# Kernel tuning notes

Hardware: AMD Instinct MI355X
Metric: run time of the kernel (lower is better)

Reference implementation:

```python
import jax, jax.numpy as jnp
import numpy as np

N_NODES = 200000
D = 512
N_EDGES = 12800000


def setup_inputs() -> dict:
    key = jax.random.key(0)
    k1, k2, k3 = jax.random.split(key, 3)
    x = jax.random.normal(k1, (N_NODES, D), dtype=jnp.float32)
    edge_index = jax.random.randint(k2, (2, N_EDGES), 0, N_NODES, dtype=jnp.int64)
    # GCNConv linear weight (glorot-ish scale) and bias
    W = jax.random.normal(k3, (D, 1), dtype=jnp.float32) / np.sqrt(D)
    b = jnp.zeros((1,), dtype=jnp.float32)
    return {"x": x, "edge_index": edge_index, "W": W, "b": b}


def reference(x, edge_index, W, b):
    """one_layer_gcn forward: GCNConv(d, 1) -> ReLU.

    Faithful to PyG GCNConv defaults: add self-loops, symmetric
    deg^{-1/2} normalization, linear transform first (out dim 1),
    scatter-add aggregation into target nodes, bias after aggregation.
    """
    n = x.shape[0]
    loop = jnp.arange(n, dtype=edge_index.dtype)
    src = jnp.concatenate([edge_index[0], loop])  # message sources (x_j)
    dst = jnp.concatenate([edge_index[1], loop])  # aggregation targets

    # degree of target nodes (with self-loops), symmetric normalization
    deg = jax.ops.segment_sum(jnp.ones_like(dst, dtype=x.dtype), dst, num_segments=n)
    dinv = jnp.where(deg > 0, jax.lax.rsqrt(deg), 0.0)
    norm = dinv[src] * dinv[dst]  # [E+N]

    h = x @ W  # [N, 1] -- trivial GEMM, out_channels = 1
    msg = h[src] * norm[:, None]  # gather + weight
    out = jax.ops.segment_sum(msg, dst, num_segments=n)  # scatter-add
    return jax.nn.relu(out + b)
```

## Files before the change

kernel.cpp:

```cpp
#include <hip/hip_runtime.h>


#define GCN_D 512
#define NPB 1024
#define NPB_SHIFT 10
#define CHUNK 8192
#define PT 512
#define CPAD 16

__global__ void init_cursor_kernel(int* __restrict__ cursor, int NB, int CAP) {
    int i = threadIdx.x;
    if (i < NB) cursor[i * CPAD] = i * CAP;
}

__global__ __launch_bounds__(PT) void place_kernel(const int* __restrict__ src,
                                                   const int* __restrict__ dst,
                                                   int* __restrict__ cursor,
                                                   unsigned int* __restrict__ packed,
                                                   int E, int NB, int CAP) {
    __shared__ unsigned int staging[CHUNK];
    __shared__ unsigned char bid[CHUNK];
    __shared__ int hist[256];
    __shared__ int lcur[256];
    __shared__ int delta[256];
    __shared__ int scanbuf[PT];

    const int tid = threadIdx.x;
    const int e0 = blockIdx.x * CHUNK;
    const int rem = min(CHUNK, E - e0);
    const int r4 = rem >> 2;

    const int4* d4p = reinterpret_cast<const int4*>(dst + e0);
    const int4* s4p = reinterpret_cast<const int4*>(src + e0);

    if (tid < 256) hist[tid] = 0;
    __syncthreads();

    int4 dreg[4];
    #pragma unroll
    for (int k = 0; k < 4; ++k) {
        int i4 = tid + k * PT;
        if (i4 < r4) {
            dreg[k] = d4p[i4];
            atomicAdd(&hist[dreg[k].x >> NPB_SHIFT], 1);
            atomicAdd(&hist[dreg[k].y >> NPB_SHIFT], 1);
            atomicAdd(&hist[dreg[k].z >> NPB_SHIFT], 1);
            atomicAdd(&hist[dreg[k].w >> NPB_SHIFT], 1);
        }
    }
    __syncthreads();

    int c = (tid < NB) ? hist[tid] : 0;
    scanbuf[tid] = c;
    for (int off = 1; off < 256; off <<= 1) {
        __syncthreads();
        int v = (tid >= off) ? scanbuf[tid - off] : 0;
        __syncthreads();
        scanbuf[tid] += v;
    }
    __syncthreads();
    if (tid < NB) {
        int ls = scanbuf[tid] - c;
        lcur[tid] = ls;
        if (c > 0)
            delta[tid] = atomicAdd(&cursor[tid * CPAD], c) - ls;
    }
    __syncthreads();

    #pragma unroll
    for (int k = 0; k < 4; ++k) {
        int i4 = tid + k * PT;
        if (i4 < r4) {
            int4 s4 = s4p[i4];
            int4 d = dreg[k];
            int b, pos;
            b = d.x >> NPB_SHIFT; pos = atomicAdd(&lcur[b], 1);
            staging[pos] = ((unsigned)s4.x << NPB_SHIFT) | (unsigned)(d.x & (NPB - 1));
            bid[pos] = (unsigned char)b;
            b = d.y >> NPB_SHIFT; pos = atomicAdd(&lcur[b], 1);
            staging[pos] = ((unsigned)s4.y << NPB_SHIFT) | (unsigned)(d.y & (NPB - 1));
            bid[pos] = (unsigned char)b;
            b = d.z >> NPB_SHIFT; pos = atomicAdd(&lcur[b], 1);
            staging[pos] = ((unsigned)s4.z << NPB_SHIFT) | (unsigned)(d.z & (NPB - 1));
            bid[pos] = (unsigned char)b;
            b = d.w >> NPB_SHIFT; pos = atomicAdd(&lcur[b], 1);
            staging[pos] = ((unsigned)s4.w << NPB_SHIFT) | (unsigned)(d.w & (NPB - 1));
            bid[pos] = (unsigned char)b;
        }
    }
    __syncthreads();

    for (int p = tid; p < rem; p += PT) {
        int b = bid[p];
        int op = p + delta[b];
        if (op < (b + 1) * CAP)
            packed[op] = staging[p];
    }
}

__global__ void gemv_kernel(const float* __restrict__ x, const float* __restrict__ W,
                            float* __restrict__ hprime, int n) {
    int wave = threadIdx.x >> 6;
    int lane = threadIdx.x & 63;
    int row = blockIdx.x * 4 + wave;
    if (row >= n) return;

    const float4* xr = reinterpret_cast<const float4*>(x + (size_t)row * GCN_D);
    const float4* Wv = reinterpret_cast<const float4*>(W);

    float4 a0 = xr[lane];
    float4 w0 = Wv[lane];
    float4 a1 = xr[lane + 64];
    float4 w1 = Wv[lane + 64];

    float dot = a0.x * w0.x + a0.y * w0.y + a0.z * w0.z + a0.w * w0.w
              + a1.x * w1.x + a1.y * w1.y + a1.z * w1.z + a1.w * w1.w;

    #pragma unroll
    for (int off = 32; off >= 1; off >>= 1)
        dot += __shfl_down(dot, off, 64);

    if (lane == 0) hprime[row] = dot;
}

__global__ __launch_bounds__(1024) void deg_hp_kernel(const unsigned int* __restrict__ packed,
                                                      const int* __restrict__ cursor,
                                                      int* __restrict__ deg,
                                                      float* __restrict__ hprime,
                                                      int N, int CAP) {
    int b = blockIdx.x;
    __shared__ int acc[NPB];
    for (int i = threadIdx.x; i < NPB; i += blockDim.x) acc[i] = 0;
    __syncthreads();
    int s0 = b * CAP;
    int s1 = min(cursor[b * CPAD], (b + 1) * CAP);
    int cnt = s1 - s0;
    int n4 = cnt >> 2;
    const uint4* p4 = reinterpret_cast<const uint4*>(packed + s0);
    for (int i = threadIdx.x; i < n4; i += blockDim.x) {
        uint4 p = p4[i];
        atomicAdd(&acc[p.x & (NPB - 1)], 1);
        atomicAdd(&acc[p.y & (NPB - 1)], 1);
        atomicAdd(&acc[p.z & (NPB - 1)], 1);
        atomicAdd(&acc[p.w & (NPB - 1)], 1);
    }
    if (threadIdx.x < (cnt & 3))
        atomicAdd(&acc[packed[s0 + (n4 << 2) + threadIdx.x] & (NPB - 1)], 1);
    __syncthreads();
    int node0 = b << NPB_SHIFT;
    for (int j = threadIdx.x; j < NPB; j += blockDim.x) {
        int node = node0 + j;
        if (node < N) {
            int dg = acc[j];
            deg[node] = dg;
            hprime[node] *= rsqrtf((float)(dg + 1));
        }
    }
}

__global__ __launch_bounds__(1024) void gather_kernel(const unsigned int* __restrict__ packed,
                                                      const int* __restrict__ cursor,
                                                      const float* __restrict__ hprime,
                                                      const int* __restrict__ deg,
                                                      const float* __restrict__ bias,
                                                      float* __restrict__ out,
                                                      int N, int CAP) {
    int b = blockIdx.x;
    __shared__ float acc[NPB];
    for (int i = threadIdx.x; i < NPB; i += blockDim.x) acc[i] = 0.f;
    __syncthreads();
    int s0 = b * CAP;
    int s1 = min(cursor[b * CPAD], (b + 1) * CAP);
    int cnt = s1 - s0;
    int n4 = cnt >> 2;
    const uint4* p4 = reinterpret_cast<const uint4*>(packed + s0);
    for (int i = threadIdx.x; i < n4; i += blockDim.x) {
        uint4 p = p4[i];
        atomicAdd(&acc[p.x & (NPB - 1)], hprime[p.x >> NPB_SHIFT]);
        atomicAdd(&acc[p.y & (NPB - 1)], hprime[p.y >> NPB_SHIFT]);
        atomicAdd(&acc[p.z & (NPB - 1)], hprime[p.z >> NPB_SHIFT]);
        atomicAdd(&acc[p.w & (NPB - 1)], hprime[p.w >> NPB_SHIFT]);
    }
    if (threadIdx.x < (cnt & 3)) {
        unsigned p = packed[s0 + (n4 << 2) + threadIdx.x];
        atomicAdd(&acc[p & (NPB - 1)], hprime[p >> NPB_SHIFT]);
    }
    __syncthreads();
    int node0 = b << NPB_SHIFT;
    float bb = bias[0];
    for (int j = threadIdx.x; j < NPB; j += blockDim.x) {
        int node = node0 + j;
        if (node < N) {
            float dinv = rsqrtf((float)(deg[node] + 1));
            float v = dinv * (acc[j] + hprime[node]) + bb;
            out[node] = v > 0.f ? v : 0.f;
        }
    }
}

__global__ void deg_kernel(const int* __restrict__ dst, int* __restrict__ deg, int e4) {
    int i = blockIdx.x * blockDim.x + threadIdx.x;
    if (i < e4) {
        int4 d = reinterpret_cast<const int4*>(dst)[i];
        atomicAdd(&deg[d.x], 1);
        atomicAdd(&deg[d.y], 1);
        atomicAdd(&deg[d.z], 1);
        atomicAdd(&deg[d.w], 1);
    }
}
__global__ void gemv_scaled_kernel(const float* __restrict__ x, const float* __restrict__ W,
                                   const int* __restrict__ deg, float* __restrict__ hprime, int n) {
    int wave = threadIdx.x >> 6;
    int lane = threadIdx.x & 63;
    int row = blockIdx.x * 4 + wave;
    if (row >= n) return;
    const float4* xr = reinterpret_cast<const float4*>(x + (size_t)row * GCN_D);
    const float4* Wv = reinterpret_cast<const float4*>(W);
    float4 a0 = xr[lane], w0 = Wv[lane];
    float4 a1 = xr[lane + 64], w1 = Wv[lane + 64];
    float dot = a0.x * w0.x + a0.y * w0.y + a0.z * w0.z + a0.w * w0.w
              + a1.x * w1.x + a1.y * w1.y + a1.z * w1.z + a1.w * w1.w;
    #pragma unroll
    for (int off = 32; off >= 1; off >>= 1) dot += __shfl_down(dot, off, 64);
    if (lane == 0) hprime[row] = dot * rsqrtf((float)(deg[row] + 1));
}
__global__ void scatter_kernel(const int* __restrict__ src, const int* __restrict__ dst,
                               const float* __restrict__ hprime, float* __restrict__ acc,
                               int e4) {
    int i = blockIdx.x * blockDim.x + threadIdx.x;
    if (i < e4) {
        int4 s = reinterpret_cast<const int4*>(src)[i];
        int4 d = reinterpret_cast<const int4*>(dst)[i];
        atomicAdd(&acc[d.x], hprime[s.x]);
        atomicAdd(&acc[d.y], hprime[s.y]);
        atomicAdd(&acc[d.z], hprime[s.z]);
        atomicAdd(&acc[d.w], hprime[s.w]);
    }
}
__global__ void final_kernel(const float* __restrict__ hprime, const float* __restrict__ acc,
                             const int* __restrict__ deg, const float* __restrict__ bptr,
                             float* __restrict__ out, int n) {
    int i = blockIdx.x * blockDim.x + threadIdx.x;
    if (i < n) {
        float dinv = rsqrtf((float)(deg[i] + 1));
        float v = dinv * (acc[i] + hprime[i]) + bptr[0];
        out[i] = v > 0.0f ? v : 0.0f;
    }
}

extern "C" void kernel_launch(void* const* d_in, const int* in_sizes, int n_in,
                              void* d_out, int out_size, void* d_ws, size_t ws_size,
                              hipStream_t stream) {
    const float* x    = (const float*)d_in[0];
    const int*   ei   = (const int*)d_in[1];
    const float* W    = (const float*)d_in[2];
    const float* bias = (const float*)d_in[3];
    float* out = (float*)d_out;

    const int n = in_sizes[0] / GCN_D;
    const int E = in_sizes[1] / 2;
    const int e4 = E / 4;

    const int* src = ei;
    const int* dst = ei + E;

    const int NB = (n + NPB - 1) >> NPB_SHIFT;

    auto align64 = [](size_t v) { return (v + 63) & ~(size_t)63; };
    size_t off_deg    = 0;
    size_t off_hprime = align64(off_deg    + (size_t)n * 4);
    size_t off_cursor = align64(off_hprime + (size_t)n * 4);
    size_t off_packed = align64(off_cursor + (size_t)NB * CPAD * 4);

    char* ws = (char*)d_ws;
    int*   deg    = (int*)(ws + off_deg);
    float* hprime = (float*)(ws + off_hprime);

    int CAP = 0;
    if (ws_size > off_packed) {
        size_t cap_avail = (ws_size - off_packed) / ((size_t)NB * 4);
        CAP = (int)(cap_avail > 131072 ? 131072 : cap_avail) & ~3;
    }
    const int mean_load = (int)(((long long)E + NB - 1) / NB);

    if (NB <= 256 && CAP >= mean_load + mean_load / 32) {
        int* cursor = (int*)(ws + off_cursor);
        unsigned int* packed = (unsigned int*)(ws + off_packed);

        init_cursor_kernel<<<1, 256, 0, stream>>>(cursor, NB, CAP);
        place_kernel<<<(E + CHUNK - 1) / CHUNK, PT, 0, stream>>>(src, dst, cursor, packed, E, NB, CAP);
        gemv_kernel<<<(n + 3) / 4, 256, 0, stream>>>(x, W, hprime, n);
        deg_hp_kernel<<<NB, 1024, 0, stream>>>(packed, cursor, deg, hprime, n, CAP);
        gather_kernel<<<NB, 1024, 0, stream>>>(packed, cursor, hprime, deg, bias, out, n, CAP);
    } else {
        float* acc = (float*)(ws + off_cursor);
        hipMemsetAsync(ws, 0, (size_t)3 * n * 4, stream);
        deg_kernel<<<(e4 + 255) / 256, 256, 0, stream>>>(dst, deg, e4);
        gemv_scaled_kernel<<<(n + 3) / 4, 256, 0, stream>>>(x, W, deg, hprime, n);
        scatter_kernel<<<(e4 + 255) / 256, 256, 0, stream>>>(src, dst, hprime, acc, e4);
        final_kernel<<<(n + 255) / 256, 256, 0, stream>>>(hprime, acc, deg, bias, out, n);
    }
}
```

Before: 249.3 us.

## Split bucket blocks across multiple CTAs and precompute placement indices in staging

The place kernel now stores each record's final global index alongside the payload in 64-bit shared staging, so the flush loop no longer looks up bucket deltas. It also uses smaller chunks with 256 threads. Degree counting and gathering now split each bucket across four 256-thread blocks that merge via global atomics into zeroed deg/accg arrays, raising parallelism over the ~196 buckets. A separate final kernel applies normalization, bias and ReLU. The GEMV processes four rows per wave and folds in the degree scaling. The cost is extra global atomics, a memset and one more launch.

New measurement: 276.9 us. +11.1%, slower.

```diff
diff --git a/kernel.cpp b/kernel.cpp
--- a/kernel.cpp
+++ b/kernel.cpp
@@ -4,9 +4,10 @@
 #define GCN_D 512
 #define NPB 1024
 #define NPB_SHIFT 10
-#define CHUNK 8192
-#define PT 512
+#define CHUNK 4096
+#define PT 256
 #define CPAD 16
+#define SPLIT 4
 
 __global__ void init_cursor_kernel(int* __restrict__ cursor, int NB, int CAP) {
     int i = threadIdx.x;
@@ -18,8 +19,7 @@
                                                    int* __restrict__ cursor,
                                                    unsigned int* __restrict__ packed,
                                                    int E, int NB, int CAP) {
-    __shared__ unsigned int staging[CHUNK];
-    __shared__ unsigned char bid[CHUNK];
+    __shared__ unsigned long long staging[CHUNK];
     __shared__ int hist[256];
     __shared__ int lcur[256];
     __shared__ int delta[256];
@@ -62,8 +62,8 @@
     if (tid < NB) {
         int ls = scanbuf[tid] - c;
         lcur[tid] = ls;
-        if (c > 0)
-            delta[tid] = atomicAdd(&cursor[tid * CPAD], c) - ls;
+        int gbase = (c > 0) ? atomicAdd(&cursor[tid * CPAD], c) : 0;
+        delta[tid] = gbase - ls;
     }
     __syncthreads();
 
@@ -73,62 +73,40 @@
         if (i4 < r4) {
             int4 s4 = s4p[i4];
             int4 d = dreg[k];
-            int b, pos;
+            int b, pos, gidx;
+            unsigned rec;
             b = d.x >> NPB_SHIFT; pos = atomicAdd(&lcur[b], 1);
-            staging[pos] = ((unsigned)s4.x << NPB_SHIFT) | (unsigned)(d.x & (NPB - 1));
-            bid[pos] = (unsigned char)b;
+            gidx = pos + delta[b]; if (gidx >= (b + 1) * CAP) gidx = (b + 1) * CAP - 1;
+            rec = ((unsigned)s4.x << NPB_SHIFT) | (unsigned)(d.x & (NPB - 1));
+            staging[pos] = ((unsigned long long)gidx << 32) | rec;
             b = d.y >> NPB_SHIFT; pos = atomicAdd(&lcur[b], 1);
-            staging[pos] = ((unsigned)s4.y << NPB_SHIFT) | (unsigned)(d.y & (NPB - 1));
-            bid[pos] = (unsigned char)b;
+            gidx = pos + delta[b]; if (gidx >= (b + 1) * CAP) gidx = (b + 1) * CAP - 1;
+            rec = ((unsigned)s4.y << NPB_SHIFT) | (unsigned)(d.y & (NPB - 1));
+            staging[pos] = ((unsigned long long)gidx << 32) | rec;
             b = d.z >> NPB_SHIFT; pos = atomicAdd(&lcur[b], 1);
-            staging[pos] = ((unsigned)s4.z << NPB_SHIFT) | (unsigned)(d.z & (NPB - 1));
-            bid[pos] = (unsigned char)b;
+            gidx = pos + delta[b]; if (gidx >= (b + 1) * CAP) gidx = (b + 1) * CAP - 1;
+            rec = ((unsigned)s4.z << NPB_SHIFT) | (unsigned)(d.z & (NPB - 1));
+            staging[pos] = ((unsigned long long)gidx << 32) | rec;
             b = d.w >> NPB_SHIFT; pos = atomicAdd(&lcur[b], 1);
-            staging[pos] = ((unsigned)s4.w << NPB_SHIFT) | (unsigned)(d.w & (NPB - 1));
-            bid[pos] = (unsigned char)b;
+            gidx = pos + delta[b]; if (gidx >= (b + 1) * CAP) gidx = (b + 1) * CAP - 1;
+            rec = ((unsigned)s4.w << NPB_SHIFT) | (unsigned)(d.w & (NPB - 1));
+            staging[pos] = ((unsigned long long)gidx << 32) | rec;
         }
     }
     __syncthreads();
 
     for (int p = tid; p < rem; p += PT) {
-        int b = bid[p];
-        int op = p + delta[b];
-        if (op < (b + 1) * CAP)
-            packed[op] = staging[p];
-    }
-}
-
-__global__ void gemv_kernel(const float* __restrict__ x, const float* __restrict__ W,
-                            float* __restrict__ hprime, int n) {
-    int wave = threadIdx.x >> 6;
-    int lane = threadIdx.x & 63;
-    int row = blockIdx.x * 4 + wave;
-    if (row >= n) return;
-
-    const float4* xr = reinterpret_cast<const float4*>(x + (size_t)row * GCN_D);
-    const float4* Wv = reinterpret_cast<const float4*>(W);
-
-    float4 a0 = xr[lane];
-    float4 w0 = Wv[lane];
-    float4 a1 = xr[lane + 64];
-    float4 w1 = Wv[lane + 64];
-
-    float dot = a0.x * w0.x + a0.y * w0.y + a0.z * w0.z + a0.w * w0.w
-              + a1.x * w1.x + a1.y * w1.y + a1.z * w1.z + a1.w * w1.w;
-
-    #pragma unroll
-    for (int off = 32; off >= 1; off >>= 1)
-        dot += __shfl_down(dot, off, 64);
-
-    if (lane == 0) hprime[row] = dot;
-}
-
-__global__ __launch_bounds__(1024) void deg_hp_kernel(const unsigned int* __restrict__ packed,
-                                                      const int* __restrict__ cursor,
-                                                      int* __restrict__ deg,
-                                                      float* __restrict__ hprime,
-                                                      int N, int CAP) {
-    int b = blockIdx.x;
+        unsigned long long v = staging[p];
+        packed[(int)(v >> 32)] = (unsigned)v;
+    }
+}
+
+__global__ __launch_bounds__(256) void deg_kernel(const unsigned int* __restrict__ packed,
+                                                  const int* __restrict__ cursor,
+                                                  int* __restrict__ deg,
+                                                  int N, int CAP) {
+    int b = blockIdx.x / SPLIT;
+    int part = blockIdx.x % SPLIT;
     __shared__ int acc[NPB];
     for (int i = threadIdx.x; i < NPB; i += blockDim.x) acc[i] = 0;
     __syncthreads();
@@ -137,35 +115,66 @@
     int cnt = s1 - s0;
     int n4 = cnt >> 2;
     const uint4* p4 = reinterpret_cast<const uint4*>(packed + s0);
-    for (int i = threadIdx.x; i < n4; i += blockDim.x) {
+    for (int i = threadIdx.x + part * blockDim.x; i < n4; i += SPLIT * blockDim.x) {
         uint4 p = p4[i];
         atomicAdd(&acc[p.x & (NPB - 1)], 1);
         atomicAdd(&acc[p.y & (NPB - 1)], 1);
         atomicAdd(&acc[p.z & (NPB - 1)], 1);
         atomicAdd(&acc[p.w & (NPB - 1)], 1);
     }
-    if (threadIdx.x < (cnt & 3))
+    if (part == 0 && threadIdx.x < (cnt & 3))
         atomicAdd(&acc[packed[s0 + (n4 << 2) + threadIdx.x] & (NPB - 1)], 1);
     __syncthreads();
     int node0 = b << NPB_SHIFT;
     for (int j = threadIdx.x; j < NPB; j += blockDim.x) {
         int node = node0 + j;
-        if (node < N) {
-            int dg = acc[j];
-            deg[node] = dg;
-            hprime[node] *= rsqrtf((float)(dg + 1));
+        if (node < N && acc[j]) atomicAdd(&deg[node], acc[j]);
+    }
+}
+
+__global__ __launch_bounds__(256) void gemv_kernel(const float* __restrict__ x,
+                                                   const float* __restrict__ W,
+                                                   const int* __restrict__ deg,
+                                                   float* __restrict__ hprime, int n) {
+    int wave = threadIdx.x >> 6;
+    int lane = threadIdx.x & 63;
+    int row0 = blockIdx.x * 16 + wave * 4;
+
+    const float4* Wv = reinterpret_cast<const float4*>(W);
+    float4 w0 = Wv[lane];
+    float4 w1 = Wv[lane + 64];
+
+    float4 a[4][2];
+    #pragma unroll
+    for (int r = 0; r < 4; ++r) {
+        int row = row0 + r;
+        if (row < n) {
+            const float4* xr = reinterpret_cast<const float4*>(x + (size_t)row * GCN_D);
+            a[r][0] = xr[lane];
+            a[r][1] = xr[lane + 64];
         }
     }
-}
-
-__global__ __launch_bounds__(1024) void gather_kernel(const unsigned int* __restrict__ packed,
-                                                      const int* __restrict__ cursor,
-                                                      const float* __restrict__ hprime,
-                                                      const int* __restrict__ deg,
-                                                      const float* __restrict__ bias,
-                                                      float* __restrict__ out,
-                                                      int N, int CAP) {
-    int b = blockIdx.x;
+    #pragma unroll
+    for (int r = 0; r < 4; ++r) {
+        int row = row0 + r;
+        if (row >= n) continue;
+        float dot = a[r][0].x * w0.x + a[r][0].y * w0.y + a[r][0].z * w0.z + a[r][0].w * w0.w
+                  + a[r][1].x * w1.x + a[r][1].y * w1.y + a[r][1].z * w1.z + a[r][1].w * w1.w;
+        #pragma unroll
+        for (int off = 32; off >= 1; off >>= 1)
+            dot += __shfl_xor(dot, off, 64);
+        if (lane == r)
+            hprime[row] = dot * rsqrtf((float)(deg[row] + 1));
+    }
+}
+
+__global__ __launch_bounds__(256) void gather_kernel(const unsigned int* __restrict__ packed,
+                                                     const int* __restrict__ cursor,
+                                                     const float* __restrict__ hprime,
+                                                     float* __restrict__ accg,
+                                                     int N, int CAP) {
+    int b = blockIdx.x / SPLIT;
+    int part = blockIdx.x % SPLIT;
     __shared__ float acc[NPB];
     for (int i = threadIdx.x; i < NPB; i += blockDim.x) acc[i] = 0.f;
     __syncthreads();
@@ -174,31 +183,37 @@
     int cnt = s1 - s0;
     int n4 = cnt >> 2;
     const uint4* p4 = reinterpret_cast<const uint4*>(packed + s0);
-    for (int i = threadIdx.x; i < n4; i += blockDim.x) {
+    for (int i = threadIdx.x + part * blockDim.x; i < n4; i += SPLIT * blockDim.x) {
         uint4 p = p4[i];
         atomicAdd(&acc[p.x & (NPB - 1)], hprime[p.x >> NPB_SHIFT]);
         atomicAdd(&acc[p.y & (NPB - 1)], hprime[p.y >> NPB_SHIFT]);
         atomicAdd(&acc[p.z & (NPB - 1)], hprime[p.z >> NPB_SHIFT]);
         atomicAdd(&acc[p.w & (NPB - 1)], hprime[p.w >> NPB_SHIFT]);
     }
-    if (threadIdx.x < (cnt & 3)) {
+    if (part == 0 && threadIdx.x < (cnt & 3)) {
         unsigned p = packed[s0 + (n4 << 2) + threadIdx.x];
         atomicAdd(&acc[p & (NPB - 1)], hprime[p >> NPB_SHIFT]);
     }
     __syncthreads();
     int node0 = b << NPB_SHIFT;
-    float bb = bias[0];
     for (int j = threadIdx.x; j < NPB; j += blockDim.x) {
         int node = node0 + j;
-        if (node < N) {
-            float dinv = rsqrtf((float)(deg[node] + 1));
-            float v = dinv * (acc[j] + hprime[node]) + bb;
-            out[node] = v > 0.f ? v : 0.f;
-        }
-    }
-}
-
-__global__ void deg_kernel(const int* __restrict__ dst, int* __restrict__ deg, int e4) {
+        if (node < N && acc[j] != 0.f) atomicAdd(&accg[node], acc[j]);
+    }
+}
+
+__global__ void final_kernel(const float* __restrict__ hprime, const float* __restrict__ accg,
+                             const int* __restrict__ deg, const float* __restrict__ bptr,
+                             float* __restrict__ out, int n) {
+    int i = blockIdx.x * blockDim.x + threadIdx.x;
+    if (i < n) {
+        float dinv = rsqrtf((float)(deg[i] + 1));
+        float v = dinv * (accg[i] + hprime[i]) + bptr[0];
+        out[i] = v > 0.0f ? v : 0.0f;
+    }
+}
+
+__global__ void deg_atomic_kernel(const int* __restrict__ dst, int* __restrict__ deg, int e4) {
     int i = blockIdx.x * blockDim.x + threadIdx.x;
     if (i < e4) {
         int4 d = reinterpret_cast<const int4*>(dst)[i];
@@ -207,22 +222,6 @@
         atomicAdd(&deg[d.z], 1);
         atomicAdd(&deg[d.w], 1);
     }
-}
-__global__ void gemv_scaled_kernel(const float* __restrict__ x, const float* __restrict__ W,
-                                   const int* __restrict__ deg, float* __restrict__ hprime, int n) {
-    int wave = threadIdx.x >> 6;
-    int lane = threadIdx.x & 63;
-    int row = blockIdx.x * 4 + wave;
-    if (row >= n) return;
-    const float4* xr = reinterpret_cast<const float4*>(x + (size_t)row * GCN_D);
-    const float4* Wv = reinterpret_cast<const float4*>(W);
-    float4 a0 = xr[lane], w0 = Wv[lane];
-    float4 a1 = xr[lane + 64], w1 = Wv[lane + 64];
-    float dot = a0.x * w0.x + a0.y * w0.y + a0.z * w0.z + a0.w * w0.w
-              + a1.x * w1.x + a1.y * w1.y + a1.z * w1.z + a1.w * w1.w;
-    #pragma unroll
-    for (int off = 32; off >= 1; off >>= 1) dot += __shfl_down(dot, off, 64);
-    if (lane == 0) hprime[row] = dot * rsqrtf((float)(deg[row] + 1));
 }
 __global__ void scatter_kernel(const int* __restrict__ src, const int* __restrict__ dst,
                                const float* __restrict__ hprime, float* __restrict__ acc,
@@ -237,16 +236,6 @@
         atomicAdd(&acc[d.w], hprime[s.w]);
     }
 }
-__global__ void final_kernel(const float* __restrict__ hprime, const float* __restrict__ acc,
-                             const int* __restrict__ deg, const float* __restrict__ bptr,
-                             float* __restrict__ out, int n) {
-    int i = blockIdx.x * blockDim.x + threadIdx.x;
-    if (i < n) {
-        float dinv = rsqrtf((float)(deg[i] + 1));
-        float v = dinv * (acc[i] + hprime[i]) + bptr[0];
-        out[i] = v > 0.0f ? v : 0.0f;
-    }
-}
 
 extern "C" void kernel_launch(void* const* d_in, const int* in_sizes, int n_in,
                               void* d_out, int out_size, void* d_ws, size_t ws_size,
@@ -268,12 +257,14 @@
 
     auto align64 = [](size_t v) { return (v + 63) & ~(size_t)63; };
     size_t off_deg    = 0;
-    size_t off_hprime = align64(off_deg    + (size_t)n * 4);
+    size_t off_accg   = align64(off_deg    + (size_t)n * 4);
+    size_t off_hprime = align64(off_accg   + (size_t)n * 4);
     size_t off_cursor = align64(off_hprime + (size_t)n * 4);
     size_t off_packed = align64(off_cursor + (size_t)NB * CPAD * 4);
 
     char* ws = (char*)d_ws;
     int*   deg    = (int*)(ws + off_deg);
+    float* accg   = (float*)(ws + off_accg);
     float* hprime = (float*)(ws + off_hprime);
 
     int CAP = 0;
@@ -287,17 +278,18 @@
         int* cursor = (int*)(ws + off_cursor);
         unsigned int* packed = (unsigned int*)(ws + off_packed);
 
+        hipMemsetAsync(ws, 0, off_hprime, stream);
         init_cursor_kernel<<<1, 256, 0, stream>>>(cursor, NB, CAP);
         place_kernel<<<(E + CHUNK - 1) / CHUNK, PT, 0, stream>>>(src, dst, cursor, packed, E, NB, CAP);
-        gemv_kernel<<<(n + 3) / 4, 256, 0, stream>>>(x, W, hprime, n);
-        deg_hp_kernel<<<NB, 1024, 0, stream>>>(packed, cursor, deg, hprime, n, CAP);
-        gather_kernel<<<NB, 1024, 0, stream>>>(packed, cursor, hprime, deg, bias, out, n, CAP);
+        deg_kernel<<<NB * SPLIT, 256, 0, stream>>>(packed, cursor, deg, n, CAP);
+        gemv_kernel<<<(n + 15) / 16, 256, 0, stream>>>(x, W, deg, hprime, n);
+        gather_kernel<<<NB * SPLIT, 256, 0, stream>>>(packed, cursor, hprime, accg, n, CAP);
+        final_kernel<<<(n + 255) / 256, 256, 0, stream>>>(hprime, accg, deg, bias, out, n);
     } else {
-        float* acc = (float*)(ws + off_cursor);
-        hipMemsetAsync(ws, 0, (size_t)3 * n * 4, stream);
-        deg_kernel<<<(e4 + 255) / 256, 256, 0, stream>>>(dst, deg, e4);
-        gemv_scaled_kernel<<<(n + 3) / 4, 256, 0, stream>>>(x, W, deg, hprime, n);
-        scatter_kernel<<<(e4 + 255) / 256, 256, 0, stream>>>(src, dst, hprime, acc, e4);
-        final_kernel<<<(n + 255) / 256, 256, 0, stream>>>(hprime, acc, deg, bias, out, n);
-    }
-}
+        hipMemsetAsync(ws, 0, off_hprime, stream);
+        deg_atomic_kernel<<<(e4 + 255) / 256, 256, 0, stream>>>(dst, deg, e4);
+        gemv_kernel<<<(n + 15) / 16, 256, 0, stream>>>(x, W, deg, hprime, n);
+        scatter_kernel<<<(e4 + 255) / 256, 256, 0, stream>>>(src, dst, hprime, accg, e4);
+        final_kernel<<<(n + 255) / 256, 256, 0, stream>>>(hprime, accg, deg, bias, out, n);
+    }
+}
```

## Fuse edge placement and GEMV into one interleaved-block kernel

Applied to the files above, without the earlier changes.

Merges the edge-bucketing place kernel and the x@W GEMV into a single launch. Place blocks are interleaved among GEMV blocks at a fixed stride, so the atomic- and LDS-heavy placement work overlaps with the bandwidth-bound streaming of x. GEMV blocks now use 512 threads and cover 8 rows each. The cost is one fewer launch and boundary, but GEMV blocks must reserve the large LDS footprint of the place path, which can lower occupancy.

Result: slower. 477.1 us (+91.4%).

```diff
diff --git a/kernel.cpp b/kernel.cpp
--- a/kernel.cpp
+++ b/kernel.cpp
@@ -5,7 +5,7 @@
 #define NPB 1024
 #define NPB_SHIFT 10
 #define CHUNK 8192
-#define PT 512
+#define FT 512
 #define CPAD 16
 
 __global__ void init_cursor_kernel(int* __restrict__ cursor, int NB, int CAP) {
@@ -13,114 +13,119 @@
     if (i < NB) cursor[i * CPAD] = i * CAP;
 }
 
-__global__ __launch_bounds__(PT) void place_kernel(const int* __restrict__ src,
-                                                   const int* __restrict__ dst,
-                                                   int* __restrict__ cursor,
-                                                   unsigned int* __restrict__ packed,
-                                                   int E, int NB, int CAP) {
+__global__ __launch_bounds__(FT) void fused_pg_kernel(
+        const int* __restrict__ src, const int* __restrict__ dst,
+        int* __restrict__ cursor, unsigned int* __restrict__ packed,
+        const float* __restrict__ x, const float* __restrict__ W,
+        float* __restrict__ hprime,
+        int E, int n, int NB, int CAP, int PB, int P) {
     __shared__ unsigned int staging[CHUNK];
-    __shared__ unsigned char bid[CHUNK];
+    __shared__ unsigned char bidb[CHUNK];
     __shared__ int hist[256];
     __shared__ int lcur[256];
     __shared__ int delta[256];
-    __shared__ int scanbuf[PT];
-
+    __shared__ int scanbuf[FT];
+
+    const int bid = blockIdx.x;
     const int tid = threadIdx.x;
-    const int e0 = blockIdx.x * CHUNK;
-    const int rem = min(CHUNK, E - e0);
-    const int r4 = rem >> 2;
-
-    const int4* d4p = reinterpret_cast<const int4*>(dst + e0);
-    const int4* s4p = reinterpret_cast<const int4*>(src + e0);
-
-    if (tid < 256) hist[tid] = 0;
-    __syncthreads();
-
-    int4 dreg[4];
-    #pragma unroll
-    for (int k = 0; k < 4; ++k) {
-        int i4 = tid + k * PT;
-        if (i4 < r4) {
-            dreg[k] = d4p[i4];
-            atomicAdd(&hist[dreg[k].x >> NPB_SHIFT], 1);
-            atomicAdd(&hist[dreg[k].y >> NPB_SHIFT], 1);
-            atomicAdd(&hist[dreg[k].z >> NPB_SHIFT], 1);
-            atomicAdd(&hist[dreg[k].w >> NPB_SHIFT], 1);
-        }
-    }
-    __syncthreads();
-
-    int c = (tid < NB) ? hist[tid] : 0;
-    scanbuf[tid] = c;
-    for (int off = 1; off < 256; off <<= 1) {
-        __syncthreads();
-        int v = (tid >= off) ? scanbuf[tid - off] : 0;
-        __syncthreads();
-        scanbuf[tid] += v;
-    }
-    __syncthreads();
-    if (tid < NB) {
-        int ls = scanbuf[tid] - c;
-        lcur[tid] = ls;
-        if (c > 0)
-            delta[tid] = atomicAdd(&cursor[tid * CPAD], c) - ls;
-    }
-    __syncthreads();
-
-    #pragma unroll
-    for (int k = 0; k < 4; ++k) {
-        int i4 = tid + k * PT;
-        if (i4 < r4) {
-            int4 s4 = s4p[i4];
-            int4 d = dreg[k];
-            int b, pos;
-            b = d.x >> NPB_SHIFT; pos = atomicAdd(&lcur[b], 1);
-            staging[pos] = ((unsigned)s4.x << NPB_SHIFT) | (unsigned)(d.x & (NPB - 1));
-            bid[pos] = (unsigned char)b;
-            b = d.y >> NPB_SHIFT; pos = atomicAdd(&lcur[b], 1);
-            staging[pos] = ((unsigned)s4.y << NPB_SHIFT) | (unsigned)(d.y & (NPB - 1));
-            bid[pos] = (unsigned char)b;
-            b = d.z >> NPB_SHIFT; pos = atomicAdd(&lcur[b], 1);
-            staging[pos] = ((unsigned)s4.z << NPB_SHIFT) | (unsigned)(d.z & (NPB - 1));
-            bid[pos] = (unsigned char)b;
-            b = d.w >> NPB_SHIFT; pos = atomicAdd(&lcur[b], 1);
-            staging[pos] = ((unsigned)s4.w << NPB_SHIFT) | (unsigned)(d.w & (NPB - 1));
-            bid[pos] = (unsigned char)b;
-        }
-    }
-    __syncthreads();
-
-    for (int p = tid; p < rem; p += PT) {
-        int b = bid[p];
-        int op = p + delta[b];
-        if (op < (b + 1) * CAP)
-            packed[op] = staging[p];
-    }
-}
-
-__global__ void gemv_kernel(const float* __restrict__ x, const float* __restrict__ W,
-                            float* __restrict__ hprime, int n) {
-    int wave = threadIdx.x >> 6;
-    int lane = threadIdx.x & 63;
-    int row = blockIdx.x * 4 + wave;
-    if (row >= n) return;
-
-    const float4* xr = reinterpret_cast<const float4*>(x + (size_t)row * GCN_D);
-    const float4* Wv = reinterpret_cast<const float4*>(W);
-
-    float4 a0 = xr[lane];
-    float4 w0 = Wv[lane];
-    float4 a1 = xr[lane + 64];
-    float4 w1 = Wv[lane + 64];
-
-    float dot = a0.x * w0.x + a0.y * w0.y + a0.z * w0.z + a0.w * w0.w
-              + a1.x * w1.x + a1.y * w1.y + a1.z * w1.z + a1.w * w1.w;
-
-    #pragma unroll
-    for (int off = 32; off >= 1; off >>= 1)
-        dot += __shfl_down(dot, off, 64);
-
-    if (lane == 0) hprime[row] = dot;
+    const bool is_place = (bid % P == 0) && (bid / P < PB);
+
+    if (is_place) {
+        const int pidx = bid / P;
+        const int e0 = pidx * CHUNK;
+        const int rem = min(CHUNK, E - e0);
+        const int r4 = rem >> 2;
+
+        const int4* d4p = reinterpret_cast<const int4*>(dst + e0);
+        const int4* s4p = reinterpret_cast<const int4*>(src + e0);
+
+        if (tid < 256) hist[tid] = 0;
+        __syncthreads();
+
+        int4 dreg[4];
+        #pragma unroll
+        for (int k = 0; k < 4; ++k) {
+            int i4 = tid + k * FT;
+            if (i4 < r4) {
+                dreg[k] = d4p[i4];
+                atomicAdd(&hist[dreg[k].x >> NPB_SHIFT], 1);
+                atomicAdd(&hist[dreg[k].y >> NPB_SHIFT], 1);
+                atomicAdd(&hist[dreg[k].z >> NPB_SHIFT], 1);
+                atomicAdd(&hist[dreg[k].w >> NPB_SHIFT], 1);
+            }
+        }
+        __syncthreads();
+
+        int c = (tid < NB) ? hist[tid] : 0;
+        scanbuf[tid] = c;
+        for (int off = 1; off < 256; off <<= 1) {
+            __syncthreads();
+            int v = (tid >= off) ? scanbuf[tid - off] : 0;
+            __syncthreads();
+            scanbuf[tid] += v;
+        }
+        __syncthreads();
+        if (tid < NB) {
+            int ls = scanbuf[tid] - c;
+            lcur[tid] = ls;
+            if (c > 0)
+                delta[tid] = atomicAdd(&cursor[tid * CPAD], c) - ls;
+        }
+        __syncthreads();
+
+        #pragma unroll
+        for (int k = 0; k < 4; ++k) {
+            int i4 = tid + k * FT;
+            if (i4 < r4) {
+                int4 s4 = s4p[i4];
+                int4 d = dreg[k];
+                int b, pos;
+                b = d.x >> NPB_SHIFT; pos = atomicAdd(&lcur[b], 1);
+                staging[pos] = ((unsigned)s4.x << NPB_SHIFT) | (unsigned)(d.x & (NPB - 1));
+                bidb[pos] = (unsigned char)b;
+                b = d.y >> NPB_SHIFT; pos = atomicAdd(&lcur[b], 1);
+                staging[pos] = ((unsigned)s4.y << NPB_SHIFT) | (unsigned)(d.y & (NPB - 1));
+                bidb[pos] = (unsigned char)b;
+                b = d.z >> NPB_SHIFT; pos = atomicAdd(&lcur[b], 1);
+                staging[pos] = ((unsigned)s4.z << NPB_SHIFT) | (unsigned)(d.z & (NPB - 1));
+                bidb[pos] = (unsigned char)b;
+                b = d.w >> NPB_SHIFT; pos = atomicAdd(&lcur[b], 1);
+                staging[pos] = ((unsigned)s4.w << NPB_SHIFT) | (unsigned)(d.w & (NPB - 1));
+                bidb[pos] = (unsigned char)b;
+            }
+        }
+        __syncthreads();
+
+        for (int p = tid; p < rem; p += FT) {
+            int b = bidb[p];
+            int op = p + delta[b];
+            if (op < (b + 1) * CAP)
+                packed[op] = staging[p];
+        }
+    } else {
+        int gidx = bid - min(bid / P + 1, PB);
+        int wave = tid >> 6;
+        int lane = tid & 63;
+        int row = gidx * 8 + wave;
+        if (row >= n) return;
+
+        const float4* xr = reinterpret_cast<const float4*>(x + (size_t)row * GCN_D);
+        const float4* Wv = reinterpret_cast<const float4*>(W);
+
+        float4 a0 = xr[lane];
+        float4 w0 = Wv[lane];
+        float4 a1 = xr[lane + 64];
+        float4 w1 = Wv[lane + 64];
+
+        float dot = a0.x * w0.x + a0.y * w0.y + a0.z * w0.z + a0.w * w0.w
+                  + a1.x * w1.x + a1.y * w1.y + a1.z * w1.z + a1.w * w1.w;
+
+        #pragma unroll
+        for (int off = 32; off >= 1; off >>= 1)
+            dot += __shfl_down(dot, off, 64);
+
+        if (lane == 0) hprime[row] = dot;
+    }
 }
 
 __global__ __launch_bounds__(1024) void deg_hp_kernel(const unsigned int* __restrict__ packed,
@@ -198,7 +203,7 @@
     }
 }
 
-__global__ void deg_kernel(const int* __restrict__ dst, int* __restrict__ deg, int e4) {
+__global__ void deg_atomic_kernel(const int* __restrict__ dst, int* __restrict__ deg, int e4) {
     int i = blockIdx.x * blockDim.x + threadIdx.x;
     if (i < e4) {
         int4 d = reinterpret_cast<const int4*>(dst)[i];
@@ -237,13 +242,13 @@
         atomicAdd(&acc[d.w], hprime[s.w]);
     }
 }
-__global__ void final_kernel(const float* __restrict__ hprime, const float* __restrict__ acc,
+__global__ void final_kernel(const float* __restrict__ hprime, const float* __restrict__ accg,
                              const int* __restrict__ deg, const float* __restrict__ bptr,
                              float* __restrict__ out, int n) {
     int i = blockIdx.x * blockDim.x + threadIdx.x;
     if (i < n) {
         float dinv = rsqrtf((float)(deg[i] + 1));
-        float v = dinv * (acc[i] + hprime[i]) + bptr[0];
+        float v = dinv * (accg[i] + hprime[i]) + bptr[0];
         out[i] = v > 0.0f ? v : 0.0f;
     }
 }
@@ -269,7 +274,8 @@
     auto align64 = [](size_t v) { return (v + 63) & ~(size_t)63; };
     size_t off_deg    = 0;
     size_t off_hprime = align64(off_deg    + (size_t)n * 4);
-    size_t off_cursor = align64(off_hprime + (size_t)n * 4);
+    size_t off_accfb  = align64(off_hprime + (size_t)n * 4);
+    size_t off_cursor = align64(off_accfb  + (size_t)n * 4);
     size_t off_packed = align64(off_cursor + (size_t)NB * CPAD * 4);
 
     char* ws = (char*)d_ws;
@@ -287,17 +293,22 @@
         int* cursor = (int*)(ws + off_cursor);
         unsigned int* packed = (unsigned int*)(ws + off_packed);
 
+        const int PB = (E + CHUNK - 1) / CHUNK;
+        const int GB = (n + 7) / 8;
+        const int R  = PB + GB;
+        int P = R / PB; if (P < 1) P = 1;
+
         init_cursor_kernel<<<1, 256, 0, stream>>>(cursor, NB, CAP);
-        place_kernel<<<(E + CHUNK - 1) / CHUNK, PT, 0, stream>>>(src, dst, cursor, packed, E, NB, CAP);
-        gemv_kernel<<<(n + 3) / 4, 256, 0, stream>>>(x, W, hprime, n);
+        fused_pg_kernel<<<R, FT, 0, stream>>>(src, dst, cursor, packed,
+                                              x, W, hprime, E, n, NB, CAP, PB, P);
         deg_hp_kernel<<<NB, 1024, 0, stream>>>(packed, cursor, deg, hprime, n, CAP);
         gather_kernel<<<NB, 1024, 0, stream>>>(packed, cursor, hprime, deg, bias, out, n, CAP);
     } else {
-        float* acc = (float*)(ws + off_cursor);
-        hipMemsetAsync(ws, 0, (size_t)3 * n * 4, stream);
-        deg_kernel<<<(e4 + 255) / 256, 256, 0, stream>>>(dst, deg, e4);
+        float* accfb = (float*)(ws + off_accfb);
+        hipMemsetAsync(ws, 0, off_cursor, stream);
+        deg_atomic_kernel<<<(e4 + 255) / 256, 256, 0, stream>>>(dst, deg, e4);
         gemv_scaled_kernel<<<(n + 3) / 4, 256, 0, stream>>>(x, W, deg, hprime, n);
-        scatter_kernel<<<(e4 + 255) / 256, 256, 0, stream>>>(src, dst, hprime, acc, e4);
-        final_kernel<<<(n + 255) / 256, 256, 0, stream>>>(hprime, acc, deg, bias, out, n);
-    }
-}
+        scatter_kernel<<<(e4 + 255) / 256, 256, 0, stream>>>(src, dst, hprime, accfb, e4);
+        final_kernel<<<(n + 255) / 256, 256, 0, stream>>>(hprime, accfb, deg, bias, out, n);
+    }
+}
```

## Replace histogram-scan binning with fixed-slot LDS buckets and global overflow

Applied to the files above, without the earlier changes.

The edge-placement kernel drops the per-block histogram, prefix scan and staged scatter. Each bucket now gets 64 fixed LDS slots, and edges that overflow go straight to global memory through per-edge global atomics. A per-wave bulk reservation then flushes each bucket. With about 196 buckets and 8192 edges per block, the expected count per bucket is about 42, so some buckets will spill to global atomics and ordering becomes scattered. The GEMV also becomes grid-stride with W held in registers, and the workspace gets a separate fallback accumulator.

Measured after the change: 277.4 us. 11.3% more time.

```diff
diff --git a/kernel.cpp b/kernel.cpp
--- a/kernel.cpp
+++ b/kernel.cpp
@@ -6,11 +6,12 @@
 #define NPB_SHIFT 10
 #define CHUNK 8192
 #define PT 512
+#define SLOTS 64
 #define CPAD 16
 
 __global__ void init_cursor_kernel(int* __restrict__ cursor, int NB, int CAP) {
-    int i = threadIdx.x;
-    if (i < NB) cursor[i * CPAD] = i * CAP;
+    for (int i = threadIdx.x; i < NB; i += blockDim.x)
+        cursor[i * CPAD] = i * CAP;
 }
 
 __global__ __launch_bounds__(PT) void place_kernel(const int* __restrict__ src,
@@ -18,12 +19,9 @@
                                                    int* __restrict__ cursor,
                                                    unsigned int* __restrict__ packed,
                                                    int E, int NB, int CAP) {
-    __shared__ unsigned int staging[CHUNK];
-    __shared__ unsigned char bid[CHUNK];
-    __shared__ int hist[256];
-    __shared__ int lcur[256];
-    __shared__ int delta[256];
-    __shared__ int scanbuf[PT];
+    extern __shared__ int smem[];
+    unsigned int* staging = (unsigned int*)smem;
+    int* lcur = smem + NB * SLOTS;
 
     const int tid = threadIdx.x;
     const int e0 = blockIdx.x * CHUNK;
@@ -33,94 +31,75 @@
     const int4* d4p = reinterpret_cast<const int4*>(dst + e0);
     const int4* s4p = reinterpret_cast<const int4*>(src + e0);
 
-    if (tid < 256) hist[tid] = 0;
-    __syncthreads();
-
-    int4 dreg[4];
+    for (int i = tid; i < NB; i += PT) lcur[i] = 0;
+    __syncthreads();
+
     #pragma unroll
     for (int k = 0; k < 4; ++k) {
         int i4 = tid + k * PT;
         if (i4 < r4) {
-            dreg[k] = d4p[i4];
-            atomicAdd(&hist[dreg[k].x >> NPB_SHIFT], 1);
-            atomicAdd(&hist[dreg[k].y >> NPB_SHIFT], 1);
-            atomicAdd(&hist[dreg[k].z >> NPB_SHIFT], 1);
-            atomicAdd(&hist[dreg[k].w >> NPB_SHIFT], 1);
-        }
-    }
-    __syncthreads();
-
-    int c = (tid < NB) ? hist[tid] : 0;
-    scanbuf[tid] = c;
-    for (int off = 1; off < 256; off <<= 1) {
-        __syncthreads();
-        int v = (tid >= off) ? scanbuf[tid - off] : 0;
-        __syncthreads();
-        scanbuf[tid] += v;
-    }
-    __syncthreads();
-    if (tid < NB) {
-        int ls = scanbuf[tid] - c;
-        lcur[tid] = ls;
-        if (c > 0)
-            delta[tid] = atomicAdd(&cursor[tid * CPAD], c) - ls;
-    }
-    __syncthreads();
-
-    #pragma unroll
-    for (int k = 0; k < 4; ++k) {
-        int i4 = tid + k * PT;
-        if (i4 < r4) {
-            int4 s4 = s4p[i4];
-            int4 d = dreg[k];
+            int4 d = d4p[i4];
+            int4 s = s4p[i4];
             int b, pos;
-            b = d.x >> NPB_SHIFT; pos = atomicAdd(&lcur[b], 1);
-            staging[pos] = ((unsigned)s4.x << NPB_SHIFT) | (unsigned)(d.x & (NPB - 1));
-            bid[pos] = (unsigned char)b;
-            b = d.y >> NPB_SHIFT; pos = atomicAdd(&lcur[b], 1);
-            staging[pos] = ((unsigned)s4.y << NPB_SHIFT) | (unsigned)(d.y & (NPB - 1));
-            bid[pos] = (unsigned char)b;
-            b = d.z >> NPB_SHIFT; pos = atomicAdd(&lcur[b], 1);
-            staging[pos] = ((unsigned)s4.z << NPB_SHIFT) | (unsigned)(d.z & (NPB - 1));
-            bid[pos] = (unsigned char)b;
-            b = d.w >> NPB_SHIFT; pos = atomicAdd(&lcur[b], 1);
-            staging[pos] = ((unsigned)s4.w << NPB_SHIFT) | (unsigned)(d.w & (NPB - 1));
-            bid[pos] = (unsigned char)b;
-        }
-    }
-    __syncthreads();
-
-    for (int p = tid; p < rem; p += PT) {
-        int b = bid[p];
-        int op = p + delta[b];
-        if (op < (b + 1) * CAP)
-            packed[op] = staging[p];
-    }
-}
-
-__global__ void gemv_kernel(const float* __restrict__ x, const float* __restrict__ W,
-                            float* __restrict__ hprime, int n) {
-    int wave = threadIdx.x >> 6;
-    int lane = threadIdx.x & 63;
-    int row = blockIdx.x * 4 + wave;
-    if (row >= n) return;
-
-    const float4* xr = reinterpret_cast<const float4*>(x + (size_t)row * GCN_D);
+            unsigned rec;
+            #define PLACE_ONE(DC, SC)                                            \
+                b = (DC) >> NPB_SHIFT;                                           \
+                rec = ((unsigned)(SC) << NPB_SHIFT) | (unsigned)((DC) & (NPB-1));\
+                pos = atomicAdd(&lcur[b], 1);                                    \
+                if (pos < SLOTS) staging[(b << 6) + pos] = rec;                  \
+                else {                       \
+                    int gp = atomicAdd(&cursor[b * CPAD], 1);                    \
+                    if (gp < (b + 1) * CAP) packed[gp] = rec;                    \
+                }
+            PLACE_ONE(d.x, s.x)
+            PLACE_ONE(d.y, s.y)
+            PLACE_ONE(d.z, s.z)
+            PLACE_ONE(d.w, s.w)
+            #undef PLACE_ONE
+        }
+    }
+    __syncthreads();
+
+    const int wid = tid >> 6;
+    const int lane = tid & 63;
+    const int nw = PT >> 6;
+    for (int b = wid; b < NB; b += nw) {
+        int cnt = lcur[b];
+        if (cnt > SLOTS) cnt = SLOTS;
+        if (cnt == 0) continue;
+        int base = 0;
+        if (lane == 0) base = atomicAdd(&cursor[b * CPAD], cnt);
+        base = __shfl(base, 0, 64);
+        if (lane < cnt) {
+            int gp = base + lane;
+            if (gp < (b + 1) * CAP)
+                packed[gp] = staging[(b << 6) + lane];
+        }
+    }
+}
+
+__global__ __launch_bounds__(1024) void gemv_kernel(const float* __restrict__ x,
+                                                    const float* __restrict__ W,
+                                                    float* __restrict__ hprime, int n) {
+    const int lane = threadIdx.x & 63;
+    const int gw = blockIdx.x * (blockDim.x >> 6) + (threadIdx.x >> 6);
+    const int stride = gridDim.x * (blockDim.x >> 6);
+
     const float4* Wv = reinterpret_cast<const float4*>(W);
-
-    float4 a0 = xr[lane];
-    float4 w0 = Wv[lane];
-    float4 a1 = xr[lane + 64];
-    float4 w1 = Wv[lane + 64];
-
-    float dot = a0.x * w0.x + a0.y * w0.y + a0.z * w0.z + a0.w * w0.w
-              + a1.x * w1.x + a1.y * w1.y + a1.z * w1.z + a1.w * w1.w;
-
-    #pragma unroll
-    for (int off = 32; off >= 1; off >>= 1)
-        dot += __shfl_down(dot, off, 64);
-
-    if (lane == 0) hprime[row] = dot;
+    const float4 w0 = Wv[lane];
+    const float4 w1 = Wv[lane + 64];
+
+    for (int row = gw; row < n; row += stride) {
+        const float4* xr = reinterpret_cast<const float4*>(x + (size_t)row * GCN_D);
+        float4 a0 = xr[lane];
+        float4 a1 = xr[lane + 64];
+        float dot = a0.x * w0.x + a0.y * w0.y + a0.z * w0.z + a0.w * w0.w
+                  + a1.x * w1.x + a1.y * w1.y + a1.z * w1.z + a1.w * w1.w;
+        #pragma unroll
+        for (int off = 32; off >= 1; off >>= 1)
+            dot += __shfl_down(dot, off, 64);
+        if (lane == 0) hprime[row] = dot;
+    }
 }
 
 __global__ __launch_bounds__(1024) void deg_hp_kernel(const unsigned int* __restrict__ packed,
@@ -198,7 +177,7 @@
     }
 }
 
-__global__ void deg_kernel(const int* __restrict__ dst, int* __restrict__ deg, int e4) {
+__global__ void deg_atomic_kernel(const int* __restrict__ dst, int* __restrict__ deg, int e4) {
     int i = blockIdx.x * blockDim.x + threadIdx.x;
     if (i < e4) {
         int4 d = reinterpret_cast<const int4*>(dst)[i];
@@ -237,13 +216,13 @@
         atomicAdd(&acc[d.w], hprime[s.w]);
     }
 }
-__global__ void final_kernel(const float* __restrict__ hprime, const float* __restrict__ acc,
+__global__ void final_kernel(const float* __restrict__ hprime, const float* __restrict__ accg,
                              const int* __restrict__ deg, const float* __restrict__ bptr,
                              float* __restrict__ out, int n) {
     int i = blockIdx.x * blockDim.x + threadIdx.x;
     if (i < n) {
         float dinv = rsqrtf((float)(deg[i] + 1));
-        float v = dinv * (acc[i] + hprime[i]) + bptr[0];
+        float v = dinv * (accg[i] + hprime[i]) + bptr[0];
         out[i] = v > 0.0f ? v : 0.0f;
     }
 }
@@ -269,7 +248,8 @@
     auto align64 = [](size_t v) { return (v + 63) & ~(size_t)63; };
     size_t off_deg    = 0;
     size_t off_hprime = align64(off_deg    + (size_t)n * 4);
-    size_t off_cursor = align64(off_hprime + (size_t)n * 4);
+    size_t off_accfb  = align64(off_hprime + (size_t)n * 4);
+    size_t off_cursor = align64(off_accfb  + (size_t)n * 4);
     size_t off_packed = align64(off_cursor + (size_t)NB * CPAD * 4);
 
     char* ws = (char*)d_ws;
@@ -282,22 +262,24 @@
         CAP = (int)(cap_avail > 131072 ? 131072 : cap_avail) & ~3;
     }
     const int mean_load = (int)(((long long)E + NB - 1) / NB);
-
-    if (NB <= 256 && CAP >= mean_load + mean_load / 32) {
+    const size_t place_lds = (size_t)(NB * SLOTS + NB) * sizeof(int);
+
+    if (NB <= 256 && CAP >= mean_load + mean_load / 32 && place_lds <= 64 * 1024) {
         int* cursor = (int*)(ws + off_cursor);
         unsigned int* packed = (unsigned int*)(ws + off_packed);
 
         init_cursor_kernel<<<1, 256, 0, stream>>>(cursor, NB, CAP);
-        place_kernel<<<(E + CHUNK - 1) / CHUNK, PT, 0, stream>>>(src, dst, cursor, packed, E, NB, CAP);
-        gemv_kernel<<<(n + 3) / 4, 256, 0, stream>>>(x, W, hprime, n);
+        place_kernel<<<(E + CHUNK - 1) / CHUNK, PT, place_lds, stream>>>(
+            src, dst, cursor, packed, E, NB, CAP);
+        gemv_kernel<<<1024, 1024, 0, stream>>>(x, W, hprime, n);
         deg_hp_kernel<<<NB, 1024, 0, stream>>>(packed, cursor, deg, hprime, n, CAP);
         gather_kernel<<<NB, 1024, 0, stream>>>(packed, cursor, hprime, deg, bias, out, n, CAP);
     } else {
-        float* acc = (float*)(ws + off_cursor);
-        hipMemsetAsync(ws, 0, (size_t)3 * n * 4, stream);
-        deg_kernel<<<(e4 + 255) / 256, 256, 0, stream>>>(dst, deg, e4);
+        float* accfb = (float*)(ws + off_accfb);
+        hipMemsetAsync(ws, 0, off_cursor, stream);
+        deg_atomic_kernel<<<(e4 + 255) / 256, 256, 0, stream>>>(dst, deg, e4);
         gemv_scaled_kernel<<<(n + 3) / 4, 256, 0, stream>>>(x, W, deg, hprime, n);
-        scatter_kernel<<<(e4 + 255) / 256, 256, 0, stream>>>(src, dst, hprime, acc, e4);
-        final_kernel<<<(n + 255) / 256, 256, 0, stream>>>(hprime, acc, deg, bias, out, n);
-    }
-}
+        scatter_kernel<<<(e4 + 255) / 256, 256, 0, stream>>>(src, dst, hprime, accfb, e4);
+        final_kernel<<<(n + 255) / 256, 256, 0, stream>>>(hprime, accfb, deg, bias, out, n);
+    }
+}
```
